# Kernel optimization log

Hardware: AMD Instinct MI355X
Metric: run time of the kernel (lower is better)

The kernel has to match this reference:

```python
import jax, jax.numpy as jnp
import numpy as np

MESH_RESOLUTION = 0.1
ORDER = 3  # TSC interpolation


def setup_inputs() -> dict:
    key = jax.random.key(0)
    k1, k2 = jax.random.split(key)
    L = 20.0
    N, C = 100000, 8
    positions = jax.random.uniform(k1, (N, 3), dtype=jnp.float32) * L
    cell = jnp.eye(3, dtype=jnp.float32) * L
    embeddings = jax.random.normal(k2, (N, C), dtype=jnp.float32)
    return {"positions": positions, "cell": cell, "embeddings": embeddings}


def _weights_order3(dist):
    # dist: [N,3]; returns [3,N,3]
    d2 = dist * dist
    return jnp.stack([
        0.125 * (1.0 - 4.0 * dist + 4.0 * d2),
        0.25 * (3.0 - 4.0 * d2),
        0.125 * (1.0 + 4.0 * dist + 4.0 * d2),
    ])


def reference(positions, cell, embeddings):
    # Mesh setup (cubic box)
    mesh_size = float(jnp.trace(cell)) / 3.0
    n_mesh = int(2 * round(mesh_size / (2.0 * MESH_RESOLUTION)))
    spacing = mesh_size / n_mesh
    C = embeddings.shape[1]

    positions_cell = positions / spacing  # [N,3]
    # odd order: nearest-grid-point centering
    idx = jnp.round(positions_cell).astype(jnp.int32)  # [N,3]
    dist = positions_cell - idx.astype(positions_cell.dtype)  # [N,3]

    w = _weights_order3(dist)  # [3,N,3]
    offs = jnp.arange(1 - (ORDER + 1) // 2, 1 + ORDER // 2)  # [-1,0,1]
    rp = (idx[None, :, :] + offs[:, None, None]) % n_mesh  # [3,N,3]

    xs, ys, zs = jnp.meshgrid(jnp.arange(ORDER), jnp.arange(ORDER), jnp.arange(ORDER), indexing='ij')
    xs, ys, zs = xs.ravel(), ys.ravel(), zs.ravel()  # [27]

    # flat grid indices and combined weights per (corner, atom)
    flat_idx = (rp[xs, :, 0] * n_mesh + rp[ys, :, 1]) * n_mesh + rp[zs, :, 2]  # [27,N]
    wprod = w[xs, :, 0] * w[ys, :, 1] * w[zs, :, 2]  # [27,N]

    vals = wprod[:, :, None] * embeddings[None, :, :]  # [27,N,C]
    grid = jnp.zeros((n_mesh ** 3, C), dtype=positions.dtype)
    grid = grid.at[flat_idx.reshape(-1)].add(vals.reshape(-1, C))
    # -> (C, n, n, n) to match mesh.values layout
    return grid.reshape(n_mesh, n_mesh, n_mesh, C).transpose(3, 0, 1, 2)
```

## Files before the change

### kernel.cpp

```cpp
#include <hip/hip_runtime.h>
#include <hip/hip_fp16.h>
#include <math.h>


#define KColCAP 16

typedef float nfloat4 __attribute__((ext_vector_type(4)));

__device__ __forceinline__ float tsc_w(int o, float d) {
    float t = 0.5f + (float)o * d;
    return (o == 0) ? (0.75f - d * d) : (0.5f * t * t);
}

__device__ __forceinline__ float inv_spacing(const float* __restrict__ cell, int n) {
    float tr = cell[0] + cell[4] + cell[8];
    return (3.0f * (float)n) / tr;
}

__device__ __forceinline__ float2 unpack_h2(float bits) {
    unsigned int u = __float_as_uint(bits);
    __half2 h = *(__half2*)&u;
    return __half22float2(h);
}


__global__ __launch_bounds__(256) void fill_recs(
    const float* __restrict__ pos, const float* __restrict__ cell,
    const float* __restrict__ emb,
    int* __restrict__ counts, int* __restrict__ ovf_cnt,
    float4* __restrict__ binrec, int* __restrict__ ovf,
    int N, int n)
{
    int i = blockIdx.x * blockDim.x + threadIdx.x;
    if (i >= N) return;
    float inv_sp = inv_spacing(cell, n);
    float px = pos[3 * i + 0] * inv_sp;
    float py = pos[3 * i + 1] * inv_sp;
    float pz = pos[3 * i + 2] * inv_sp;
    int cx = (int)rintf(px); if (cx >= n) cx -= n; else if (cx < 0) cx += n;
    int cy = (int)rintf(py); if (cy >= n) cy -= n; else if (cy < 0) cy += n;
    int bin = cx * n + cy;
    int slot = atomicAdd(&counts[bin], 1);
    if (slot < KColCAP) {
        const float4* e4 = (const float4*)(emb + (size_t)i * 8);
        float4 e0 = e4[0], e1 = e4[1];
        __half2 h01 = __floats2half2_rn(e0.x, e0.y);
        __half2 h23 = __floats2half2_rn(e0.z, e0.w);
        __half2 h45 = __floats2half2_rn(e1.x, e1.y);
        __half2 h67 = __floats2half2_rn(e1.z, e1.w);
        unsigned int u01 = *(unsigned int*)&h01;
        unsigned int u23 = *(unsigned int*)&h23;
        unsigned int u45 = *(unsigned int*)&h45;
        unsigned int u67 = *(unsigned int*)&h67;
        float4* r = binrec + (size_t)(bin * KColCAP + slot) * 2;
        r[0] = make_float4(px, py, pz, __uint_as_float(u01));
        r[1] = make_float4(__uint_as_float(u23), __uint_as_float(u45),
                           __uint_as_float(u67), 0.0f);
    } else {
        int o = atomicAdd(ovf_cnt, 1);
        ovf[o] = i;
    }
}


__global__ __launch_bounds__(256) void gather_scatter(
    const float4* __restrict__ binrec, const int* __restrict__ counts,
    float* __restrict__ out, int n, int nzc)
{
    extern __shared__ float lds[];
    const int tid = threadIdx.x;
    const int lane = tid & 63;
    const int wv = tid >> 6;

    const int nb = nzc * n;
    const int b = blockIdx.x;
    const int q8 = nb >> 3, r8 = nb & 7;
    const int xcd = b & 7, idx = b >> 3;
    const int sb = (xcd < r8) ? (xcd * (q8 + 1) + idx)
                              : (r8 * (q8 + 1) + (xcd - r8) * q8 + idx);
    const int x = sb / nzc;
    const int ygrp = sb - x * nzc;
    const int y = ygrp * 4 + wv;

    float* col = lds + wv * 8 * n;

    {
        nfloat4* c4 = (nfloat4*)col;
        const int z4 = 2 * n;
        for (int i = lane; i < z4; i += 64)
            c4[i] = (nfloat4)(0.f);
    }

    int base[9], pref[10];
    pref[0] = 0;
    #pragma unroll
    for (int j = 0; j < 9; ++j) {
        int jx = j / 3, jy = j - 3 * (j / 3);
        int xb = x + jx - 1; if (xb < 0) xb += n; else if (xb >= n) xb -= n;
        int yb = y + jy - 1; if (yb < 0) yb += n; else if (yb >= n) yb -= n;
        int bin = xb * n + yb;
        base[j] = bin * KColCAP;
        int c = counts[bin];
        c = (c < KColCAP) ? c : KColCAP;
        pref[j + 1] = pref[j] + c;
    }
    const int tot = pref[9];

    const int s  = lane / 3;
    const int zc = lane - 3 * s - 1;

    float4 a0, a1; int jxA = 0, jyA = 0;
    bool vA = (s < 21) && (s < tot);
    if (vA) {
        int rec = base[0] + s; int jxv = 0, jyv = 0;
        #pragma unroll
        for (int k = 1; k < 9; ++k) {
            bool ge = (s >= pref[k]);
            int cand = base[k] + (s - pref[k]);
            rec = ge ? cand : rec;
            jxv = ge ? (k / 3) : jxv;
            jyv = ge ? (k - 3 * (k / 3)) : jyv;
        }
        a0 = binrec[2 * (size_t)rec];
        a1 = binrec[2 * (size_t)rec + 1];
        jxA = jxv; jyA = jyv;
    }

    for (int q0 = 0; q0 < tot; q0 += 21) {
        const int qn = q0 + 21 + s;
        const bool vB = (s < 21) && (qn < tot);
        float4 b0 = a0, b1 = a1; int jxB = jxA, jyB = jyA;
        if (vB) {
            int rec = base[0] + qn; int jxv = 0, jyv = 0;
            #pragma unroll
            for (int k = 1; k < 9; ++k) {
                bool ge = (qn >= pref[k]);
                int cand = base[k] + (qn - pref[k]);
                rec = ge ? cand : rec;
                jxv = ge ? (k / 3) : jxv;
                jyv = ge ? (k - 3 * (k / 3)) : jyv;
            }
            b0 = binrec[2 * (size_t)rec];
            b1 = binrec[2 * (size_t)rec + 1];
            jxB = jxv; jyB = jyv;
        }

        if (vA) {
            float cxf = rintf(a0.x); float dx = a0.x - cxf;
            float cyf = rintf(a0.y); float dy = a0.y - cyf;
            float czf = rintf(a0.z); float dz = a0.z - czf;

            float tx = 0.5f + (float)(1 - jxA) * dx;
            float wx = (jxA == 1) ? (0.75f - dx * dx) : (0.5f * tx * tx);
            float ty = 0.5f + (float)(1 - jyA) * dy;
            float wy = (jyA == 1) ? (0.75f - dy * dy) : (0.5f * ty * ty);
            float tz = 0.5f + (float)zc * dz;
            float wz = (zc == 0) ? (0.75f - dz * dz) : (0.5f * tz * tz);
            float w = wx * wy * wz;

            float2 e01 = unpack_h2(a0.w);
            float2 e23 = unpack_h2(a1.x);
            float2 e45 = unpack_h2(a1.y);
            float2 e67 = unpack_h2(a1.z);

            int cz = (int)czf; if (cz >= n) cz -= n; else if (cz < 0) cz += n;
            int z = cz + zc; if (z < 0) z += n; else if (z >= n) z -= n;

            float* p = col + z;
            atomicAdd(p + 0 * n, w * e01.x);
            atomicAdd(p + 1 * n, w * e01.y);
            atomicAdd(p + 2 * n, w * e23.x);
            atomicAdd(p + 3 * n, w * e23.y);
            atomicAdd(p + 4 * n, w * e45.x);
            atomicAdd(p + 5 * n, w * e45.y);
            atomicAdd(p + 6 * n, w * e67.x);
            atomicAdd(p + 7 * n, w * e67.y);
        }
        a0 = b0; a1 = b1; jxA = jxB; jyA = jyB; vA = vB;
    }

    const int z0 = lane * 4;
    if (z0 < n) {
        const size_t n3 = (size_t)n * n * n;
        const size_t colbase = ((size_t)x * n + y) * (size_t)n + z0;
        #pragma unroll
        for (int ch = 0; ch < 8; ++ch) {
            nfloat4 v = *(const nfloat4*)(col + ch * n + z0);
            *(nfloat4*)(out + (size_t)ch * n3 + colbase) = v;
        }
    }
}

__global__ __launch_bounds__(256) void deposit_overflow(
    const float* __restrict__ pos, const float* __restrict__ cell,
    const float* __restrict__ emb, const int* __restrict__ ovf_cnt,
    const int* __restrict__ ovf, float* __restrict__ out, int n)
{
    int m = *ovf_cnt;
    int i = blockIdx.x * blockDim.x + threadIdx.x;
    if (i >= m) return;
    int ai = ovf[i];
    float inv_sp = inv_spacing(cell, n);
    float p[3], d[3]; int c0[3];
    #pragma unroll
    for (int kk = 0; kk < 3; ++kk) {
        p[kk] = pos[3 * ai + kk] * inv_sp;
        c0[kk] = (int)rintf(p[kk]);
        d[kk] = p[kk] - (float)c0[kk];
    }
    float w[3][3];
    #pragma unroll
    for (int kk = 0; kk < 3; ++kk) {
        float dd = d[kk];
        w[kk][0] = tsc_w(-1, dd); w[kk][1] = tsc_w(0, dd); w[kk][2] = tsc_w(1, dd);
    }
    int W[3][3];
    #pragma unroll
    for (int kk = 0; kk < 3; ++kk)
        #pragma unroll
        for (int a = 0; a < 3; ++a) {
            int v = c0[kk] - 1 + a; if (v < 0) v += n; else if (v >= n) v -= n;
            W[kk][a] = v;
        }
    size_t n3 = (size_t)n * n * n;
    const float4* e4 = (const float4*)(emb + (size_t)ai * 8);
    float4 e0 = e4[0], e1 = e4[1];
    float e[8] = {e0.x, e0.y, e0.z, e0.w, e1.x, e1.y, e1.z, e1.w};
    for (int a = 0; a < 3; ++a)
        for (int bq = 0; bq < 3; ++bq)
            for (int cq = 0; cq < 3; ++cq) {
                float wt = w[0][a] * w[1][bq] * w[2][cq];
                size_t g = ((size_t)W[0][a] * n + W[1][bq]) * n + W[2][cq];
                #pragma unroll
                for (int ch = 0; ch < 8; ++ch)
                    atomicAdd(out + (size_t)ch * n3 + g, wt * e[ch]);
            }
}


__global__ __launch_bounds__(256) void deposit_tsc8_ilv(
    const float* __restrict__ pos,
    const float* __restrict__ cell,
    const float* __restrict__ emb,
    float* __restrict__ ws,
    int total, int n)
{
    int t = blockIdx.x * blockDim.x + threadIdx.x;
    if (t >= total) return;
    int atom = t / 27;
    int c    = t - atom * 27;
    int a    = c / 9;
    int rem  = c - a * 9;
    int b    = rem / 3;
    int cc   = rem - b * 3;

    float inv_sp = inv_spacing(cell, n);

    float px = pos[3 * atom + 0] * inv_sp;
    float py = pos[3 * atom + 1] * inv_sp;
    float pz = pos[3 * atom + 2] * inv_sp;

    int cx = (int)rintf(px);  float dx = px - (float)cx;
    int cy = (int)rintf(py);  float dy = py - (float)cy;
    int cz = (int)rintf(pz);  float dz = pz - (float)cz;

    float w = tsc_w(a - 1, dx) * tsc_w(b - 1, dy) * tsc_w(cc - 1, dz);

    int x = cx - 1 + a;  if (x < 0) x += n; else if (x >= n) x -= n;
    int y = cy - 1 + b;  if (y < 0) y += n; else if (y >= n) y -= n;
    int z = cz - 1 + cc; if (z < 0) z += n; else if (z >= n) z -= n;

    const float4* e4 = (const float4*)(emb + (size_t)atom * 8);
    float4 e0 = e4[0], e1 = e4[1];

    float* p = ws + ((size_t)((x * n + y) * n + z)) * 8;
    atomicAdd(p + 0, w * e0.x);
    atomicAdd(p + 1, w * e0.y);
    atomicAdd(p + 2, w * e0.z);
    atomicAdd(p + 3, w * e0.w);
    atomicAdd(p + 4, w * e1.x);
    atomicAdd(p + 5, w * e1.y);
    atomicAdd(p + 6, w * e1.z);
    atomicAdd(p + 7, w * e1.w);
}

__global__ __launch_bounds__(256) void transpose_ilv8(
    const float* __restrict__ ws, float* __restrict__ out, int n3)
{
    int t = blockIdx.x * blockDim.x + threadIdx.x;
    int g0 = t * 4;
    if (g0 >= n3) return;
    const float4* w4 = (const float4*)(ws + (size_t)g0 * 8);
    float4 r0 = w4[0], r1 = w4[1];
    float4 r2 = w4[2], r3 = w4[3];
    float4 r4 = w4[4], r5 = w4[5];
    float4 r6 = w4[6], r7 = w4[7];

    *(float4*)(out + (size_t)0 * n3 + g0) = make_float4(r0.x, r2.x, r4.x, r6.x);
    *(float4*)(out + (size_t)1 * n3 + g0) = make_float4(r0.y, r2.y, r4.y, r6.y);
    *(float4*)(out + (size_t)2 * n3 + g0) = make_float4(r0.z, r2.z, r4.z, r6.z);
    *(float4*)(out + (size_t)3 * n3 + g0) = make_float4(r0.w, r2.w, r4.w, r6.w);
    *(float4*)(out + (size_t)4 * n3 + g0) = make_float4(r1.x, r3.x, r5.x, r7.x);
    *(float4*)(out + (size_t)5 * n3 + g0) = make_float4(r1.y, r3.y, r5.y, r7.y);
    *(float4*)(out + (size_t)6 * n3 + g0) = make_float4(r1.z, r3.z, r5.z, r7.z);
    *(float4*)(out + (size_t)7 * n3 + g0) = make_float4(r1.w, r3.w, r5.w, r7.w);
}


__global__ __launch_bounds__(256) void deposit_tsc_gen(
    const float* __restrict__ pos,
    const float* __restrict__ cell,
    const float* __restrict__ emb,
    float* __restrict__ out,
    int N, int n, int C)
{
    int i = blockIdx.x * blockDim.x + threadIdx.x;
    if (i >= N) return;

    float inv_sp = inv_spacing(cell, n);

    float p[3], d[3];
    int c0[3];
    #pragma unroll
    for (int k = 0; k < 3; ++k) {
        p[k] = pos[3 * i + k] * inv_sp;
        c0[k] = (int)rintf(p[k]);
        d[k] = p[k] - (float)c0[k];
    }
    float w[3][3];
    #pragma unroll
    for (int k = 0; k < 3; ++k) {
        float dd = d[k], d2 = dd * dd;
        w[k][0] = 0.125f * (1.0f - 4.0f * dd + 4.0f * d2);
        w[k][1] = 0.25f  * (3.0f - 4.0f * d2);
        w[k][2] = 0.125f * (1.0f + 4.0f * dd + 4.0f * d2);
    }
    int W[3][3];
    #pragma unroll
    for (int k = 0; k < 3; ++k) {
        #pragma unroll
        for (int a = 0; a < 3; ++a) {
            int v = c0[k] - 1 + a; if (v < 0) v += n; else if (v >= n) v -= n;
            W[k][a] = v;
        }
    }
    int n3 = n * n * n;
    for (int a = 0; a < 3; ++a)
        for (int b = 0; b < 3; ++b)
            for (int cc = 0; cc < 3; ++cc) {
                float wt = w[0][a] * w[1][b] * w[2][cc];
                int g = (W[0][a] * n + W[1][b]) * n + W[2][cc];
                for (int ch = 0; ch < C; ++ch)
                    atomicAdd(out + (size_t)ch * n3 + g, wt * emb[(size_t)i * C + ch]);
            }
}

extern "C" void kernel_launch(void* const* d_in, const int* in_sizes, int n_in,
                              void* d_out, int out_size, void* d_ws, size_t ws_size,
                              hipStream_t stream) {
    const float* pos  = (const float*)d_in[0];
    const float* cell = (const float*)d_in[1];
    const float* emb  = (const float*)d_in[2];
    float* out = (float*)d_out;
    float* ws  = (float*)d_ws;

    int N = in_sizes[0] / 3;
    int C = in_sizes[2] / N;
    long long n3l = (long long)out_size / C;
    int n = (int)llroundf(cbrtf((float)n3l));
    int n3 = (int)n3l;

    int block = 256;

    {
        int nb = n * n;
        size_t lds_bytes = (size_t)4 * 8 * n * sizeof(float);
        size_t rec_off = (((size_t)nb + 4 + (size_t)N) * sizeof(int) + 15) & ~(size_t)15;
        size_t need = rec_off + (size_t)nb * KColCAP * 32;
        bool ok = (C == 8) && (n % 4 == 0) && n >= 8 && n <= 256
                  && lds_bytes <= 64 * 1024
                  && ws_size >= need
                  && ((long long)n * n * n == n3l);
        if (ok) {
            int* counts  = (int*)d_ws;
            int* ovf_cnt = counts + nb;
            int* ovf     = counts + nb + 4;
            float4* binrec = (float4*)((char*)d_ws + rec_off);

            (void)hipMemsetAsync(counts, 0, (size_t)(nb + 4) * sizeof(int), stream);
            fill_recs<<<(N + block - 1) / block, block, 0, stream>>>(
                pos, cell, emb, counts, ovf_cnt, binrec, ovf, N, n);

            int nzc = n / 4;
            gather_scatter<<<nzc * n, block, lds_bytes, stream>>>(
                binrec, counts, out, n, nzc);

            deposit_overflow<<<(N + block - 1) / block, block, 0, stream>>>(
                pos, cell, emb, ovf_cnt, ovf, out, n);
            return;
        }
    }

    size_t need = (size_t)out_size * sizeof(float);
    if (C == 8 && ws_size >= need && (n3 % 4) == 0) {
        (void)hipMemsetAsync(d_ws, 0, need, stream);
        int total = N * 27;
        deposit_tsc8_ilv<<<(total + block - 1) / block, block, 0, stream>>>(
            pos, cell, emb, ws, total, n);
        int tthreads = n3 / 4;
        transpose_ilv8<<<(tthreads + block - 1) / block, block, 0, stream>>>(
            ws, out, n3);
    } else {
        (void)hipMemsetAsync(d_out, 0, (size_t)out_size * sizeof(float), stream);
        int grid = (N + block - 1) / block;
        deposit_tsc_gen<<<grid, block, 0, stream>>>(pos, cell, emb, out, N, n, C);
    }
}
```

Before: 145.7 us.

## Use persistent blocks looping over column tiles and replace memset with zero kernel

```diff
diff --git a/kernel.cpp b/kernel.cpp
--- a/kernel.cpp
+++ b/kernel.cpp
@@ -21,6 +21,14 @@
     unsigned int u = __float_as_uint(bits);
     __half2 h = *(__half2*)&u;
     return __half22float2(h);
+}
+
+
+__global__ __launch_bounds__(256) void zero_ints(int* __restrict__ p, int nwords)
+{
+    int i = blockIdx.x * blockDim.x + threadIdx.x;
+    int stride = gridDim.x * blockDim.x;
+    for (int k = i; k < nwords; k += stride) p[k] = 0;
 }
 
 
@@ -65,128 +73,106 @@
 
 __global__ __launch_bounds__(256) void gather_scatter(
     const float4* __restrict__ binrec, const int* __restrict__ counts,
-    float* __restrict__ out, int n, int nzc)
+    float* __restrict__ out, int n, int nzc, int tpb)
 {
     extern __shared__ float lds[];
     const int tid = threadIdx.x;
     const int lane = tid & 63;
     const int wv = tid >> 6;
-
     const int nb = nzc * n;
-    const int b = blockIdx.x;
-    const int q8 = nb >> 3, r8 = nb & 7;
-    const int xcd = b & 7, idx = b >> 3;
-    const int sb = (xcd < r8) ? (xcd * (q8 + 1) + idx)
-                              : (r8 * (q8 + 1) + (xcd - r8) * q8 + idx);
-    const int x = sb / nzc;
-    const int ygrp = sb - x * nzc;
-    const int y = ygrp * 4 + wv;
+    const size_t n3 = (size_t)n * n * n;
 
     float* col = lds + wv * 8 * n;
 
-    {
-        nfloat4* c4 = (nfloat4*)col;
-        const int z4 = 2 * n;
-        for (int i = lane; i < z4; i += 64)
-            c4[i] = (nfloat4)(0.f);
-    }
-
-    int base[9], pref[10];
-    pref[0] = 0;
-    #pragma unroll
-    for (int j = 0; j < 9; ++j) {
-        int jx = j / 3, jy = j - 3 * (j / 3);
-        int xb = x + jx - 1; if (xb < 0) xb += n; else if (xb >= n) xb -= n;
-        int yb = y + jy - 1; if (yb < 0) yb += n; else if (yb >= n) yb -= n;
-        int bin = xb * n + yb;
-        base[j] = bin * KColCAP;
-        int c = counts[bin];
-        c = (c < KColCAP) ? c : KColCAP;
-        pref[j + 1] = pref[j] + c;
-    }
-    const int tot = pref[9];
-
-    const int s  = lane / 3;
-    const int zc = lane - 3 * s - 1;
-
-    float4 a0, a1; int jxA = 0, jyA = 0;
-    bool vA = (s < 21) && (s < tot);
-    if (vA) {
-        int rec = base[0] + s; int jxv = 0, jyv = 0;
+    int t0 = blockIdx.x * tpb;
+    int t1 = t0 + tpb; if (t1 > nb) t1 = nb;
+
+    for (int t = t0; t < t1; ++t) {
+        const int x = t / nzc;
+        const int ygrp = t - x * nzc;
+        const int y = ygrp * 4 + wv;
+
+        {
+            nfloat4* c4 = (nfloat4*)col;
+            const int z4 = 2 * n;
+            for (int i = lane; i < z4; i += 64)
+                c4[i] = (nfloat4)(0.f);
+        }
+
+        int base[9], pref[10];
+        pref[0] = 0;
         #pragma unroll
-        for (int k = 1; k < 9; ++k) {
-            bool ge = (s >= pref[k]);
-            int cand = base[k] + (s - pref[k]);
-            rec = ge ? cand : rec;
-            jxv = ge ? (k / 3) : jxv;
-            jyv = ge ? (k - 3 * (k / 3)) : jyv;
-        }
-        a0 = binrec[2 * (size_t)rec];
-        a1 = binrec[2 * (size_t)rec + 1];
-        jxA = jxv; jyA = jyv;
-    }
-
-    for (int q0 = 0; q0 < tot; q0 += 21) {
-        const int qn = q0 + 21 + s;
-        const bool vB = (s < 21) && (qn < tot);
-        float4 b0 = a0, b1 = a1; int jxB = jxA, jyB = jyA;
-        if (vB) {
-            int rec = base[0] + qn; int jxv = 0, jyv = 0;
+        for (int j = 0; j < 9; ++j) {
+            int jx = j / 3, jy = j - 3 * (j / 3);
+            int xb = x + jx - 1; if (xb < 0) xb += n; else if (xb >= n) xb -= n;
+            int yb = y + jy - 1; if (yb < 0) yb += n; else if (yb >= n) yb -= n;
+            int bin = xb * n + yb;
+            base[j] = bin * KColCAP;
+            int c = counts[bin];
+            c = (c < KColCAP) ? c : KColCAP;
+            pref[j + 1] = pref[j] + c;
+        }
+        const int tot = pref[9];
+
+        const int s  = lane / 3;
+        const int zc = lane - 3 * s - 1;
+
+        for (int q0 = 0; q0 < tot; q0 += 21) {
+            const int qq = q0 + s;
+            if (s < 21 && qq < tot) {
+                int rec = base[0] + qq;
+                int jxv = 0, jyv = 0;
+                #pragma unroll
+                for (int k = 1; k < 9; ++k) {
+                    bool ge = (qq >= pref[k]);
+                    int cand = base[k] + (qq - pref[k]);
+                    rec = ge ? cand : rec;
+                    jxv = ge ? (k / 3) : jxv;
+                    jyv = ge ? (k - 3 * (k / 3)) : jyv;
+                }
+                float4 a0 = binrec[2 * (size_t)rec];
+                float4 a1 = binrec[2 * (size_t)rec + 1];
+
+                float cxf = rintf(a0.x); float dx = a0.x - cxf;
+                float cyf = rintf(a0.y); float dy = a0.y - cyf;
+                float czf = rintf(a0.z); float dz = a0.z - czf;
+
+                float tx = 0.5f + (float)(1 - jxv) * dx;
+                float wx = (jxv == 1) ? (0.75f - dx * dx) : (0.5f * tx * tx);
+                float ty = 0.5f + (float)(1 - jyv) * dy;
+                float wy = (jyv == 1) ? (0.75f - dy * dy) : (0.5f * ty * ty);
+                float tz = 0.5f + (float)zc * dz;
+                float wz = (zc == 0) ? (0.75f - dz * dz) : (0.5f * tz * tz);
+                float w = wx * wy * wz;
+
+                float2 e01 = unpack_h2(a0.w);
+                float2 e23 = unpack_h2(a1.x);
+                float2 e45 = unpack_h2(a1.y);
+                float2 e67 = unpack_h2(a1.z);
+
+                int cz = (int)czf; if (cz >= n) cz -= n; else if (cz < 0) cz += n;
+                int z = cz + zc; if (z < 0) z += n; else if (z >= n) z -= n;
+
+                float* p = col + z;
+                atomicAdd(p + 0 * n, w * e01.x);
+                atomicAdd(p + 1 * n, w * e01.y);
+                atomicAdd(p + 2 * n, w * e23.x);
+                atomicAdd(p + 3 * n, w * e23.y);
+                atomicAdd(p + 4 * n, w * e45.x);
+                atomicAdd(p + 5 * n, w * e45.y);
+                atomicAdd(p + 6 * n, w * e67.x);
+                atomicAdd(p + 7 * n, w * e67.y);
+            }
+        }
+
+        const int z0 = lane * 4;
+        if (z0 < n) {
+            const size_t colbase = ((size_t)x * n + y) * (size_t)n + z0;
             #pragma unroll
-            for (int k = 1; k < 9; ++k) {
-                bool ge = (qn >= pref[k]);
-                int cand = base[k] + (qn - pref[k]);
-                rec = ge ? cand : rec;
-                jxv = ge ? (k / 3) : jxv;
-                jyv = ge ? (k - 3 * (k / 3)) : jyv;
+            for (int ch = 0; ch < 8; ++ch) {
+                nfloat4 v = *(const nfloat4*)(col + ch * n + z0);
+                *(nfloat4*)(out + (size_t)ch * n3 + colbase) = v;
             }
-            b0 = binrec[2 * (size_t)rec];
-            b1 = binrec[2 * (size_t)rec + 1];
-            jxB = jxv; jyB = jyv;
-        }
-
-        if (vA) {
-            float cxf = rintf(a0.x); float dx = a0.x - cxf;
-            float cyf = rintf(a0.y); float dy = a0.y - cyf;
-            float czf = rintf(a0.z); float dz = a0.z - czf;
-
-            float tx = 0.5f + (float)(1 - jxA) * dx;
-            float wx = (jxA == 1) ? (0.75f - dx * dx) : (0.5f * tx * tx);
-            float ty = 0.5f + (float)(1 - jyA) * dy;
-            float wy = (jyA == 1) ? (0.75f - dy * dy) : (0.5f * ty * ty);
-            float tz = 0.5f + (float)zc * dz;
-            float wz = (zc == 0) ? (0.75f - dz * dz) : (0.5f * tz * tz);
-            float w = wx * wy * wz;
-
-            float2 e01 = unpack_h2(a0.w);
-            float2 e23 = unpack_h2(a1.x);
-            float2 e45 = unpack_h2(a1.y);
-            float2 e67 = unpack_h2(a1.z);
-
-            int cz = (int)czf; if (cz >= n) cz -= n; else if (cz < 0) cz += n;
-            int z = cz + zc; if (z < 0) z += n; else if (z >= n) z -= n;
-
-            float* p = col + z;
-            atomicAdd(p + 0 * n, w * e01.x);
-            atomicAdd(p + 1 * n, w * e01.y);
-            atomicAdd(p + 2 * n, w * e23.x);
-            atomicAdd(p + 3 * n, w * e23.y);
-            atomicAdd(p + 4 * n, w * e45.x);
-            atomicAdd(p + 5 * n, w * e45.y);
-            atomicAdd(p + 6 * n, w * e67.x);
-            atomicAdd(p + 7 * n, w * e67.y);
-        }
-        a0 = b0; a1 = b1; jxA = jxB; jyA = jyB; vA = vB;
-    }
-
-    const int z0 = lane * 4;
-    if (z0 < n) {
-        const size_t n3 = (size_t)n * n * n;
-        const size_t colbase = ((size_t)x * n + y) * (size_t)n + z0;
-        #pragma unroll
-        for (int ch = 0; ch < 8; ++ch) {
-            nfloat4 v = *(const nfloat4*)(col + ch * n + z0);
-            *(nfloat4*)(out + (size_t)ch * n3 + colbase) = v;
         }
     }
 }
@@ -387,13 +373,17 @@
             int* ovf     = counts + nb + 4;
             float4* binrec = (float4*)((char*)d_ws + rec_off);
 
-            (void)hipMemsetAsync(counts, 0, (size_t)(nb + 4) * sizeof(int), stream);
+            zero_ints<<<256, block, 0, stream>>>(counts, nb + 4);
             fill_recs<<<(N + block - 1) / block, block, 0, stream>>>(
                 pos, cell, emb, counts, ovf_cnt, binrec, ovf, N, n);
 
             int nzc = n / 4;
-            gather_scatter<<<nzc * n, block, lds_bytes, stream>>>(
-                binrec, counts, out, n, nzc);
+            int nbt = nzc * n;
+            int nblocks = 2500;
+            if (nblocks > nbt) nblocks = nbt;
+            int tpb = (nbt + nblocks - 1) / nblocks;
+            gather_scatter<<<nblocks, block, lds_bytes, stream>>>(
+                binrec, counts, out, n, nzc, tpb);
 
             deposit_overflow<<<(N + block - 1) / block, block, 0, stream>>>(
                 pos, cell, emb, ovf_cnt, ovf, out, n);
```

After: 152.9 us. 1.05x slower.
